# Kernel optimization log

Measured on AMD Instinct MI355X. Metric: run time of the kernel, lower is better.

## Reference

```python
import jax, jax.numpy as jnp
import numpy as np

B, N = 16, 262144          # batch, pixels per image (512*512)
N_CLASSES = 150            # ADE20K-like
N_PRED = 4096              # global predicted segment ids


def setup_inputs() -> dict:
    key = jax.random.key(0)
    k1, k2 = jax.random.split(key)
    predseg = jax.random.randint(k1, (B, N), 0, N_PRED, dtype=jnp.int64)
    targetseg = jax.random.randint(k2, (B, N), 0, N_CLASSES, dtype=jnp.int64)
    # eye buffer from the module (self._targets), treated as a float param
    targets = jnp.eye(N_CLASSES, dtype=jnp.float32)
    return {
        "predseg": predseg,
        "targetseg": targetseg,
        "targets": targets,
        "n_classes": N_CLASSES,
        "n_pred_ids": N_PRED,
    }


def reference(predseg, targetseg, targets, n_classes, n_pred_ids):
    b, n = predseg.shape
    T = b * n_classes  # number of distinct target segment ids (b_idx*maxseg + class)
    pred = predseg.reshape(-1)
    # target id = batch_index * n_classes + class label, exactly as in torch
    tgt = (jnp.arange(b, dtype=predseg.dtype)[:, None] * n_classes + targetseg).reshape(-1)

    # Dense co-occurrence histogram O[p, t] = #pixels with pred==p and target==t.
    # Equivalent to the sort/unique pipeline: pairs with O==0 had IoU contribution 0.
    flat = pred * T + tgt
    O = jnp.zeros((n_pred_ids * T,), jnp.float32).at[flat].add(1.0)
    O = O.reshape(n_pred_ids, T)

    n_pred = O.sum(axis=1, keepdims=True)    # pixels per pred segment
    n_tgt = O.sum(axis=0, keepdims=True)     # pixels per target segment
    iou = jnp.where(O > 0, O / (n_pred + n_tgt - O), 0.0)  # [P, B*C]

    # scatter_reduce of iou * targets[class] over pred ids ==
    # sum over batch then matmul with the class-target matrix
    iou_pc = iou.reshape(n_pred_ids, b, n_classes).sum(axis=1)  # [P, C]
    out = iou_pc @ targets                                      # [P, C]
    den = out.sum(axis=-1, keepdims=True)
    return out / den
```

## Files before the change

kernel.cpp:

```cpp
#include <hip/hip_runtime.h>

#define B_    16
#define N_    262144
#define NC    150
#define NP    4096
#define T_    (B_ * NC)
#define TOTAL (B_ * N_)

#define PBKT       256
#define PCAP       18432
#define KEY_SHIFT  16
#define P1_BLOCKS  1024
#define P1_PIX     (TOTAL / P1_BLOCKS)
#define P1_PER_THR (P1_PIX / 256)

#define QT         9600

#define CSTRIDE    64
#define NCOUNTERS  (PBKT * CSTRIDE + T_)

typedef unsigned int u32;
typedef unsigned short u16;

__global__ __launch_bounds__(256) void init_kernel(u32* __restrict__ ctrs) {
    int i = blockIdx.x * 256 + threadIdx.x;
    if (i < NCOUNTERS) ctrs[i] = 0;
}

__global__ __launch_bounds__(256) void partition_kernel(const int* __restrict__ pred,
                                                        const int* __restrict__ tgt,
                                                        u16* __restrict__ records,
                                                        u32* __restrict__ gCount,
                                                        u32* __restrict__ gNT) {
    __shared__ u32 cnt[PBKT];
    __shared__ u32 lstart[PBKT];
    __shared__ u32 goff[PBKT];
    __shared__ u32 cursor[PBKT];
    __shared__ u32 nth[NC];
    __shared__ u32 wsum[4];
    __shared__ u32 staging[P1_PIX];

    int tid = threadIdx.x;
    cnt[tid] = 0;
    if (tid < NC) nth[tid] = 0;

    int base = blockIdx.x * P1_PIX;
    int b_img = base >> 18;
    const int4* pred4 = (const int4*)pred;
    const int4* tgt4  = (const int4*)tgt;
    int4 pv[4], tv[4];
    #pragma unroll
    for (int k = 0; k < 4; ++k) {
        int vi = (base >> 2) + k * 256 + tid;
        pv[k] = pred4[vi];
        tv[k] = tgt4[vi];
    }
    __syncthreads();

    u32 keys[P1_PER_THR];
    #pragma unroll
    for (int k = 0; k < 4; ++k) {
        int pe[4] = {pv[k].x, pv[k].y, pv[k].z, pv[k].w};
        int te[4] = {tv[k].x, tv[k].y, tv[k].z, tv[k].w};
        #pragma unroll
        for (int e = 0; e < 4; ++e) {
            int p = pe[e];
            u32 bkt = (u32)(p >> 4);
            u32 lk  = (u32)((p & 15) * T_ + b_img * NC + te[e]);
            keys[k * 4 + e] = (bkt << KEY_SHIFT) | lk;
            atomicAdd(&cnt[bkt], 1u);
            atomicAdd(&nth[te[e]], 1u);
        }
    }
    __syncthreads();

    {
        u32 myc = cnt[tid];
        u32 v = myc;
        #pragma unroll
        for (int o = 1; o < 64; o <<= 1) {
            u32 t = __shfl_up(v, o);
            if ((tid & 63) >= o) v += t;
        }
        if ((tid & 63) == 63) wsum[tid >> 6] = v;
        __syncthreads();
        u32 woff = 0;
        #pragma unroll
        for (int w = 0; w < 3; ++w) woff += (w < (tid >> 6)) ? wsum[w] : 0;
        u32 ex = v + woff - myc;
        lstart[tid] = ex;
        cursor[tid] = ex;
        u32 gb = atomicAdd(&gCount[tid * CSTRIDE], myc);
        goff[tid] = gb - ex;
    }
    if (tid < NC && nth[tid]) atomicAdd(&gNT[b_img * NC + tid], nth[tid]);
    __syncthreads();

    #pragma unroll
    for (int k = 0; k < P1_PER_THR; ++k) {
        u32 v = keys[k];
        u32 pos = atomicAdd(&cursor[v >> KEY_SHIFT], 1u);
        staging[pos] = v;
    }
    __syncthreads();

    for (int r = tid; r < P1_PIX; r += 256) {
        u32 v = staging[r];
        u32 bkt = v >> KEY_SHIFT;
        u32 gp = goff[bkt] + (u32)r;
        if (gp < PCAP) records[(size_t)bkt * PCAP + gp] = (u16)(v & 0xFFFFu);
    }
}

__global__ __launch_bounds__(256, 6) void iou_kernel(const u16* __restrict__ records,
                                                     const u32* __restrict__ gCount,
                                                     const u32* __restrict__ gNT,
                                                     const float* __restrict__ targets,
                                                     float* __restrict__ out) {
    __shared__ u32 hist[QT / 2];
    __shared__ float npred_s[4];
    __shared__ float iou_pc[4][NC];
    __shared__ float4 red4[256];

    int tid = threadIdx.x;
    int bkt = blockIdx.x & 255;
    int q   = blockIdx.x >> 8;
    u32 lo = (u32)(q * QT);

    {
        uint4 z4 = make_uint4(0u, 0u, 0u, 0u);
        uint4* h4 = (uint4*)hist;
        for (int j = tid; j < QT / 8; j += 256) h4[j] = z4;
    }
    __syncthreads();

    u32 cnt = gCount[bkt * CSTRIDE];
    if (cnt > PCAP) cnt = PCAP;
    const u16* rec = records + (size_t)bkt * PCAP;

    u32 nv4 = cnt >> 2;
    const ushort4* rec4 = (const ushort4*)rec;
    {
        u32 r = tid;
        ushort4 cur;
        if (r < nv4) cur = rec4[r];
        for (; r < nv4; ) {
            u32 rn = r + 256;
            ushort4 nxt;
            if (rn < nv4) nxt = rec4[rn];
            u32 e[4] = {cur.x, cur.y, cur.z, cur.w};
            #pragma unroll
            for (int i = 0; i < 4; ++i) {
                u32 lk = e[i] - lo;
                if (lk < (u32)QT)
                    atomicAdd(&hist[lk >> 1], (lk & 1u) ? 65536u : 1u);
            }
            cur = nxt;
            r = rn;
        }
    }
    for (u32 r = (nv4 << 2) + tid; r < cnt; r += 256) {
        u32 lk = (u32)rec[r] - lo;
        if (lk < (u32)QT)
            atomicAdd(&hist[lk >> 1], (lk & 1u) ? 65536u : 1u);
    }
    __syncthreads();

    {
        int pl = tid >> 6, lane = tid & 63;
        u32 s = 0;
        for (int w = lane; w < T_ / 2; w += 64) {
            u32 v = hist[pl * (T_ / 2) + w];
            s += (v & 0xFFFFu) + (v >> 16);
        }
        #pragma unroll
        for (int o = 32; o > 0; o >>= 1) s += __shfl_xor(s, o);
        if (lane == 0) npred_s[pl] = (float)s;
    }
    __syncthreads();

    for (int idx = tid; idx < 4 * NC; idx += 256) {
        int pl = idx / NC, cls = idx - pl * NC;
        float np = npred_s[pl];
        float acc = 0.f;
        #pragma unroll
        for (int b = 0; b < B_; ++b) {
            int lk = pl * T_ + b * NC + cls;
            u32 w = hist[lk >> 1];
            u32 v = (lk & 1) ? (w >> 16) : (w & 0xFFFFu);
            if (v) {
                float fv = (float)v;
                acc += fv * __builtin_amdgcn_rcpf(np + (float)gNT[b * NC + cls] - fv);
            }
        }
        iou_pc[pl][cls] = acc;
    }
    __syncthreads();

    float o0 = 0.f, o1 = 0.f, o2 = 0.f, o3 = 0.f;
    if (tid < NC) {
        for (int k = 0; k < NC; ++k) {
            float tv = targets[k * NC + tid];
            o0 += iou_pc[0][k] * tv;
            o1 += iou_pc[1][k] * tv;
            o2 += iou_pc[2][k] * tv;
            o3 += iou_pc[3][k] * tv;
        }
    }

    red4[tid] = (tid < NC) ? make_float4(o0, o1, o2, o3)
                           : make_float4(0.f, 0.f, 0.f, 0.f);
    __syncthreads();
    for (int o = 128; o > 0; o >>= 1) {
        if (tid < o) {
            float4 a = red4[tid], b = red4[tid + o];
            red4[tid] = make_float4(a.x + b.x, a.y + b.y, a.z + b.z, a.w + b.w);
        }
        __syncthreads();
    }
    float4 den = red4[0];

    if (tid < NC) {
        size_t ob = (size_t)(bkt * 16 + q * 4) * NC + tid;
        out[ob + 0 * NC] = o0 * __builtin_amdgcn_rcpf(den.x);
        out[ob + 1 * NC] = o1 * __builtin_amdgcn_rcpf(den.y);
        out[ob + 2 * NC] = o2 * __builtin_amdgcn_rcpf(den.z);
        out[ob + 3 * NC] = o3 * __builtin_amdgcn_rcpf(den.w);
    }
}

extern "C" void kernel_launch(void* const* d_in, const int* in_sizes, int n_in,
                              void* d_out, int out_size, void* d_ws, size_t ws_size,
                              hipStream_t stream) {
    const int*   pred    = (const int*)d_in[0];
    const int*   tgt     = (const int*)d_in[1];
    const float* targets = (const float*)d_in[2];
    float*       out     = (float*)d_out;

    u32* gCount  = (u32*)d_ws;
    u32* gNT     = gCount + PBKT * CSTRIDE;
    u16* records = (u16*)(gNT + T_);

    init_kernel<<<(NCOUNTERS + 255) / 256, 256, 0, stream>>>((u32*)d_ws);
    partition_kernel<<<P1_BLOCKS, 256, 0, stream>>>(pred, tgt, records, gCount, gNT);
    iou_kernel<<<PBKT * 4, 256, 0, stream>>>(records, gCount, gNT, targets, out);
}
```

Measured before the change: 60.24 us.

## Split work finer and privatize per-wave shared counters in partition

```diff
diff --git a/kernel.cpp b/kernel.cpp
--- a/kernel.cpp
+++ b/kernel.cpp
@@ -10,11 +10,13 @@
 #define PBKT       256
 #define PCAP       18432
 #define KEY_SHIFT  16
-#define P1_BLOCKS  1024
+#define P1_BLOCKS  2048
 #define P1_PIX     (TOTAL / P1_BLOCKS)
 #define P1_PER_THR (P1_PIX / 256)
 
-#define QT         9600
+#define SUBQ       8
+#define QP         2
+#define QT         (QP * T_)
 
 #define CSTRIDE    64
 #define NCOUNTERS  (PBKT * CSTRIDE + T_)
@@ -27,30 +29,34 @@
     if (i < NCOUNTERS) ctrs[i] = 0;
 }
 
-__global__ __launch_bounds__(256) void partition_kernel(const int* __restrict__ pred,
-                                                        const int* __restrict__ tgt,
-                                                        u16* __restrict__ records,
-                                                        u32* __restrict__ gCount,
-                                                        u32* __restrict__ gNT) {
-    __shared__ u32 cnt[PBKT];
+__global__ __launch_bounds__(256, 8) void partition_kernel(const int* __restrict__ pred,
+                                                           const int* __restrict__ tgt,
+                                                           u16* __restrict__ records,
+                                                           u32* __restrict__ gCount,
+                                                           u32* __restrict__ gNT) {
+    __shared__ u32 cnt4[4][PBKT];
     __shared__ u32 lstart[PBKT];
     __shared__ u32 goff[PBKT];
-    __shared__ u32 cursor[PBKT];
-    __shared__ u32 nth[NC];
+    __shared__ u32 nth4[4][160];
     __shared__ u32 wsum[4];
     __shared__ u32 staging[P1_PIX];
 
     int tid = threadIdx.x;
-    cnt[tid] = 0;
-    if (tid < NC) nth[tid] = 0;
+    int w   = tid >> 6;
+    #pragma unroll
+    for (int i = 0; i < 4; ++i) cnt4[i][tid] = 0;
+    if (tid < 160) {
+        #pragma unroll
+        for (int i = 0; i < 4; ++i) nth4[i][tid] = 0;
+    }
 
     int base = blockIdx.x * P1_PIX;
     int b_img = base >> 18;
     const int4* pred4 = (const int4*)pred;
     const int4* tgt4  = (const int4*)tgt;
-    int4 pv[4], tv[4];
-    #pragma unroll
-    for (int k = 0; k < 4; ++k) {
+    int4 pv[2], tv[2];
+    #pragma unroll
+    for (int k = 0; k < 2; ++k) {
         int vi = (base >> 2) + k * 256 + tid;
         pv[k] = pred4[vi];
         tv[k] = tgt4[vi];
@@ -59,7 +65,7 @@
 
     u32 keys[P1_PER_THR];
     #pragma unroll
-    for (int k = 0; k < 4; ++k) {
+    for (int k = 0; k < 2; ++k) {
         int pe[4] = {pv[k].x, pv[k].y, pv[k].z, pv[k].w};
         int te[4] = {tv[k].x, tv[k].y, tv[k].z, tv[k].w};
         #pragma unroll
@@ -68,38 +74,45 @@
             u32 bkt = (u32)(p >> 4);
             u32 lk  = (u32)((p & 15) * T_ + b_img * NC + te[e]);
             keys[k * 4 + e] = (bkt << KEY_SHIFT) | lk;
-            atomicAdd(&cnt[bkt], 1u);
-            atomicAdd(&nth[te[e]], 1u);
-        }
-    }
-    __syncthreads();
-
-    {
-        u32 myc = cnt[tid];
+            atomicAdd(&cnt4[w][bkt], 1u);
+            atomicAdd(&nth4[w][te[e]], 1u);
+        }
+    }
+    __syncthreads();
+
+    {
+        u32 c0 = cnt4[0][tid], c1 = cnt4[1][tid], c2 = cnt4[2][tid], c3 = cnt4[3][tid];
+        u32 myc = c0 + c1 + c2 + c3;
         u32 v = myc;
         #pragma unroll
         for (int o = 1; o < 64; o <<= 1) {
             u32 t = __shfl_up(v, o);
             if ((tid & 63) >= o) v += t;
         }
-        if ((tid & 63) == 63) wsum[tid >> 6] = v;
+        if ((tid & 63) == 63) wsum[w] = v;
         __syncthreads();
         u32 woff = 0;
         #pragma unroll
-        for (int w = 0; w < 3; ++w) woff += (w < (tid >> 6)) ? wsum[w] : 0;
+        for (int ww = 0; ww < 3; ++ww) woff += (ww < w) ? wsum[ww] : 0;
         u32 ex = v + woff - myc;
         lstart[tid] = ex;
-        cursor[tid] = ex;
+        cnt4[0][tid] = ex;
+        cnt4[1][tid] = ex + c0;
+        cnt4[2][tid] = ex + c0 + c1;
+        cnt4[3][tid] = ex + c0 + c1 + c2;
         u32 gb = atomicAdd(&gCount[tid * CSTRIDE], myc);
         goff[tid] = gb - ex;
     }
-    if (tid < NC && nth[tid]) atomicAdd(&gNT[b_img * NC + tid], nth[tid]);
+    if (tid < NC) {
+        u32 s = nth4[0][tid] + nth4[1][tid] + nth4[2][tid] + nth4[3][tid];
+        if (s) atomicAdd(&gNT[b_img * NC + tid], s);
+    }
     __syncthreads();
 
     #pragma unroll
     for (int k = 0; k < P1_PER_THR; ++k) {
         u32 v = keys[k];
-        u32 pos = atomicAdd(&cursor[v >> KEY_SHIFT], 1u);
+        u32 pos = atomicAdd(&cnt4[w][v >> KEY_SHIFT], 1u);
         staging[pos] = v;
     }
     __syncthreads();
@@ -112,15 +125,15 @@
     }
 }
 
-__global__ __launch_bounds__(256, 6) void iou_kernel(const u16* __restrict__ records,
+__global__ __launch_bounds__(256, 8) void iou_kernel(const u16* __restrict__ records,
                                                      const u32* __restrict__ gCount,
                                                      const u32* __restrict__ gNT,
                                                      const float* __restrict__ targets,
                                                      float* __restrict__ out) {
     __shared__ u32 hist[QT / 2];
-    __shared__ float npred_s[4];
-    __shared__ float iou_pc[4][NC];
-    __shared__ float4 red4[256];
+    __shared__ float npred_part[4];
+    __shared__ float iou_pc[QP][NC];
+    __shared__ float2 red2[256];
 
     int tid = threadIdx.x;
     int bkt = blockIdx.x & 255;
@@ -167,21 +180,21 @@
     __syncthreads();
 
     {
-        int pl = tid >> 6, lane = tid & 63;
+        int pl = tid >> 7, lane128 = tid & 127;
         u32 s = 0;
-        for (int w = lane; w < T_ / 2; w += 64) {
-            u32 v = hist[pl * (T_ / 2) + w];
+        for (int wd = lane128; wd < T_ / 2; wd += 128) {
+            u32 v = hist[pl * (T_ / 2) + wd];
             s += (v & 0xFFFFu) + (v >> 16);
         }
         #pragma unroll
         for (int o = 32; o > 0; o >>= 1) s += __shfl_xor(s, o);
-        if (lane == 0) npred_s[pl] = (float)s;
-    }
-    __syncthreads();
-
-    for (int idx = tid; idx < 4 * NC; idx += 256) {
+        if ((tid & 63) == 0) npred_part[tid >> 6] = (float)s;
+    }
+    __syncthreads();
+
+    for (int idx = tid; idx < QP * NC; idx += 256) {
         int pl = idx / NC, cls = idx - pl * NC;
-        float np = npred_s[pl];
+        float np = npred_part[2 * pl] + npred_part[2 * pl + 1];
         float acc = 0.f;
         #pragma unroll
         for (int b = 0; b < B_; ++b) {
@@ -197,35 +210,30 @@
     }
     __syncthreads();
 
-    float o0 = 0.f, o1 = 0.f, o2 = 0.f, o3 = 0.f;
+    float o0 = 0.f, o1 = 0.f;
     if (tid < NC) {
         for (int k = 0; k < NC; ++k) {
             float tv = targets[k * NC + tid];
             o0 += iou_pc[0][k] * tv;
             o1 += iou_pc[1][k] * tv;
-            o2 += iou_pc[2][k] * tv;
-            o3 += iou_pc[3][k] * tv;
-        }
-    }
-
-    red4[tid] = (tid < NC) ? make_float4(o0, o1, o2, o3)
-                           : make_float4(0.f, 0.f, 0.f, 0.f);
+        }
+    }
+
+    red2[tid] = (tid < NC) ? make_float2(o0, o1) : make_float2(0.f, 0.f);
     __syncthreads();
     for (int o = 128; o > 0; o >>= 1) {
         if (tid < o) {
-            float4 a = red4[tid], b = red4[tid + o];
-            red4[tid] = make_float4(a.x + b.x, a.y + b.y, a.z + b.z, a.w + b.w);
+            float2 a = red2[tid], b = red2[tid + o];
+            red2[tid] = make_float2(a.x + b.x, a.y + b.y);
         }
         __syncthreads();
     }
-    float4 den = red4[0];
+    float2 den = red2[0];
 
     if (tid < NC) {
-        size_t ob = (size_t)(bkt * 16 + q * 4) * NC + tid;
+        size_t ob = (size_t)(bkt * 16 + q * QP) * NC + tid;
         out[ob + 0 * NC] = o0 * __builtin_amdgcn_rcpf(den.x);
         out[ob + 1 * NC] = o1 * __builtin_amdgcn_rcpf(den.y);
-        out[ob + 2 * NC] = o2 * __builtin_amdgcn_rcpf(den.z);
-        out[ob + 3 * NC] = o3 * __builtin_amdgcn_rcpf(den.w);
     }
 }
 
@@ -243,5 +251,5 @@
 
     init_kernel<<<(NCOUNTERS + 255) / 256, 256, 0, stream>>>((u32*)d_ws);
     partition_kernel<<<P1_BLOCKS, 256, 0, stream>>>(pred, tgt, records, gCount, gNT);
-    iou_kernel<<<PBKT * 4, 256, 0, stream>>>(records, gCount, gNT, targets, out);
-}
+    iou_kernel<<<PBKT * SUBQ, 256, 0, stream>>>(records, gCount, gNT, targets, out);
+}
```

New measurement: 74.11 us. 23.0% more time.
